# Kernel optimization log

Measured on AMD Instinct MI355X. Metric: run time of the kernel, lower is better.

## Reference

```python
import jax, jax.numpy as jnp
import numpy as np

ALPHA = 0.9
NEG_SLOPE = 0.01  # nn.LeakyReLU default
PAD = 1           # circular padding

def _conv_circular(t, W, b):
    # circular pad spatial dims, then VALID conv (matches padding_mode='circular')
    tp = jnp.pad(t, ((0, 0), (0, 0), (PAD, PAD), (PAD, PAD)), mode='wrap')
    y = jax.lax.conv_general_dilated(
        tp, W, window_strides=(1, 1), padding='VALID',
        dimension_numbers=('NCHW', 'OIHW', 'NCHW'))
    return y + b[None, :, None, None]

def setup_inputs() -> dict:
    key = jax.random.key(0)
    k1, k2, k3, k4 = jax.random.split(key, 4)
    x = jax.random.normal(k1, (32, 64, 56, 56), dtype=jnp.float32)
    n = jax.random.normal(k2, (32, 64, 56, 56), dtype=jnp.float32)
    fan_in = 64 * 3 * 3
    W = jax.random.normal(k3, (256, 64, 3, 3), dtype=jnp.float32) / np.sqrt(fan_in)
    b = jax.random.normal(k4, (256,), dtype=jnp.float32) * 0.01
    return {"x": x, "n": n, "W": W, "b": b}

def reference(x, n, W, b):
    h1 = _conv_circular(x, W, b)            # [B, N, C, F]
    hn = _conv_circular(n, W, b)            # [B, N, C, F]
    B, N, C, F = h1.shape
    xf = h1.reshape(B, N, C * F)            # tran(x) again == h1
    nf = hn.reshape(B, N, C * F)
    a = jnp.einsum('bnf,bmf->bnm', xf, nf)  # [B, N, M]
    a = jnp.where(a >= 0, a, NEG_SLOPE * a) # LeakyReLU
    attn = jax.nn.softmax(a, axis=1)        # Softmax(dim=1): over rows
    agg = jnp.einsum('bnm,bmf->bnf', attn, xf).reshape(B, N, C, F)
    return (1.0 - ALPHA) * agg + ALPHA * h1
```

## Files before the change

kernel.cpp:

```cpp
#include <hip/hip_runtime.h>
#include <hip/hip_bf16.h>
#include <cstddef>

#define SP 3136
#define CIN 64
#define COUT 256
#define NB 32
#define NEG_SLOPE 0.01f

typedef __attribute__((ext_vector_type(8))) short short8v;
typedef __attribute__((ext_vector_type(4))) float f32x4;

__device__ __forceinline__ float bfr(ushort h) {
    union { uint u; float f; } c; c.u = ((uint)h) << 16; return c.f;
}
__device__ __forceinline__ ushort bf_hi(float v) {
    __hip_bfloat16 h = __float2bfloat16(v);
    return *(ushort*)&h;
}

#define SWZ(row, g) ((((g) ^ ((row) & 7))) * 8)

#define GLOAD_LDS(gp, lp) __builtin_amdgcn_global_load_lds(                    \
    (const __attribute__((address_space(1))) void*)(gp),                       \
    (__attribute__((address_space(3))) void*)(lp), 16, 0, 0)

__global__ __launch_bounds__(256)
void pack_w(const float* __restrict__ W, ushort* __restrict__ wh)
{
    const int id = blockIdx.x * 256 + threadIdx.x;
    const int ci = id & 63, co = (id >> 6) & 255, tap = id >> 14;
    float v = W[(size_t)(co * 64 + ci) * 9 + tap];
    const int ks = ci >> 5, cig = (ci >> 3) & 3, ce = ci & 7;
    const size_t o = (((size_t)(tap * 2 + ks) * 4 + cig) * 256 + co) * 8 + ce;
    wh[o] = bf_hi(v);
}

__global__ __launch_bounds__(256, 2)
void conv_fused(const float* __restrict__ xsrc, const float* __restrict__ nsrc,
                const ushort* __restrict__ Wf_hi,
                const float* __restrict__ bias,
                ushort* __restrict__ h1h, ushort* __restrict__ hnh)
{
    __shared__ __align__(16) ushort Bh[4 * 58 * 64];
    const int tid = threadIdx.x;
    const int w = tid >> 6, l = tid & 63;
    const int bid = blockIdx.x;
    const int xcd = bid & 7, s = bid >> 3;
    const int rp  = s % 28;
    const int img = xcd + 8 * (s / 28);
    const int imgb = img & (NB - 1);
    const int y0 = rp * 2, p0 = rp * 112;
    const int co_w = w * 64;
    const bool isX = (img < NB);

    const float* __restrict__ src = (isX ? xsrc : nsrc) + (size_t)imgb * CIN * SP;
    ushort* __restrict__ dh = (isX ? h1h : hnh) + (size_t)imgb * COUT * SP;

    int sy[4];
    #pragma unroll
    for (int j = 0; j < 4; ++j) sy[j] = (y0 + 55 + j) % 56;

    {
        const int ci = tid >> 2, seg = tid & 3;
        #pragma unroll
        for (int j = 0; j < 4; ++j) {
            const float* r = src + (size_t)ci * SP + sy[j] * 56 + seg * 14;
            #pragma unroll
            for (int c = 0; c < 14; ++c) {
                const int x = seg * 14 + c + 1;
                const int idx = ((j * 58 + x) << 6) + (((ci >> 3) ^ (x & 7)) << 3) + (ci & 7);
                Bh[idx] = bf_hi(r[c]);
            }
        }
        #pragma unroll
        for (int s2 = 0; s2 < 2; ++s2) {
            const int slot = tid * 2 + s2;
            const int j2 = slot >> 7, ci2 = (slot >> 1) & 63, side = slot & 1;
            const float* r2 = src + (size_t)ci2 * SP + sy[j2] * 56;
            const float v = side ? r2[0] : r2[55];
            const int x = side ? 57 : 0;
            const int idx = ((j2 * 58 + x) << 6) + (((ci2 >> 3) ^ (x & 7)) << 3) + (ci2 & 7);
            Bh[idx] = bf_hi(v);
        }
    }
    __syncthreads();

    f32x4 acc[4][7];
    {
        const int rr = (l >> 4) * 4;
        #pragma unroll
        for (int m = 0; m < 4; ++m) {
            const int cb = co_w + 16 * m + rr;
            f32x4 bv = { bias[cb], bias[cb + 1], bias[cb + 2], bias[cb + 3] };
            #pragma unroll
            for (int nf = 0; nf < 7; ++nf) acc[m][nf] = bv;
        }
    }

    int b58[7], bx[7];
    #pragma unroll
    for (int nf = 0; nf < 7; ++nf) {
        const int sp = nf * 16 + (l & 15);
        const int ry = (sp >= 56) ? 1 : 0;
        const int xx = sp - ry * 56;
        b58[nf] = ry * 58 + xx;
        bx[nf]  = xx;
    }

    size_t aoff[4];
    #pragma unroll
    for (int m = 0; m < 4; ++m)
        aoff[m] = ((size_t)(l >> 4) * 256 + co_w + 16 * m + (l & 15)) * 8;

    short8v cah[4];
    #pragma unroll
    for (int m = 0; m < 4; ++m)
        cah[m] = *(const short8v*)(Wf_hi + aoff[m]);

    for (int it = 0; it < 18; ++it) {
        const int tap = it >> 1, ks = it & 1;
        const int dy = tap / 3, dx = tap - dy * 3;
        const int toff = dy * 58 + dx;
        const int grp = ks * 4 + (l >> 4);

        short8v nah[4];
        {
            const size_t po = (size_t)(it < 17 ? it + 1 : it) * 8192;
            #pragma unroll
            for (int m = 0; m < 4; ++m)
                nah[m] = *(const short8v*)(Wf_hi + aoff[m] + po);
        }

        #pragma unroll
        for (int nf = 0; nf < 7; ++nf) {
            const int x  = bx[nf] + dx;
            const int bi = ((b58[nf] + toff) << 6) + ((grp ^ (x & 7)) << 3);
            short8v bh = *(const short8v*)&Bh[bi];
            #pragma unroll
            for (int m = 0; m < 4; ++m)
                acc[m][nf] = __builtin_amdgcn_mfma_f32_16x16x32_bf16(cah[m], bh, acc[m][nf], 0, 0, 0);
        }
        #pragma unroll
        for (int m = 0; m < 4; ++m) cah[m] = nah[m];
    }

    const int rr = (l >> 4) * 4, cc = l & 15;
    #pragma unroll
    for (int m = 0; m < 4; ++m) {
        const int cb = co_w + 16 * m + rr;
        #pragma unroll
        for (int nf = 0; nf < 7; ++nf) {
            const int p = p0 + nf * 16 + cc;
            #pragma unroll
            for (int r = 0; r < 4; ++r)
                dh[(size_t)(cb + r) * SP + p] = bf_hi(acc[m][nf][r]);
        }
    }
}

__global__ __launch_bounds__(256, 2)
void gemm_a_mfma(const ushort* __restrict__ h1h, const ushort* __restrict__ hnh,
                 float* __restrict__ attn)
{
    __shared__ __align__(16) ushort Ah[64][64];
    __shared__ __align__(16) ushort Bh[64][64];
    const int tid = threadIdx.x;
    const int w = tid >> 6, l = tid & 63;
    const int wn = w >> 1, wm = w & 1;
    const int bid = blockIdx.x;
    const int xcd = bid & 7, s = bid >> 3;
    const int tile = s % 16;
    const int img  = xcd + 8 * (s / 16);
    const int n0 = (tile & 3) * 64, m0 = (tile >> 2) * 64;

    const ushort* __restrict__ mat0 = h1h + ((size_t)img * COUT + n0) * SP;
    const ushort* __restrict__ mat1 = hnh + ((size_t)img * COUT + m0) * SP;

    f32x4 acc[2][2];
    #pragma unroll
    for (int i = 0; i < 2; ++i)
        #pragma unroll
        for (int j = 0; j < 2; ++j) acc[i][j] = (f32x4){0.f, 0.f, 0.f, 0.f};

    const int lr = l >> 3, gp = l & 7;
    const int glog = gp ^ lr;
    const ushort* gptr[4];
    ushort* lptr[4];
    #pragma unroll
    for (int t = 0; t < 4; ++t) {
        const int u = 4 * w + t, mat = u >> 3, seg = u & 7;
        const ushort* ms = (mat == 0) ? mat0 : mat1;
        ushort* lb = (mat == 0) ? &Ah[0][0] : &Bh[0][0];
        gptr[t] = ms + (size_t)(seg * 8 + lr) * SP + glog * 8;
        lptr[t] = lb + seg * 8 * 64;
    }

    for (int k0 = 0; k0 < SP; k0 += 64) {
        #pragma unroll
        for (int t = 0; t < 4; ++t)
            GLOAD_LDS(gptr[t] + k0, lptr[t]);
        __syncthreads();

        #pragma unroll
        for (int ks = 0; ks < 2; ++ks) {
            const int grp = ks * 4 + (l >> 4);
            short8v ahf[2], bhf[2];
            #pragma unroll
            for (int i = 0; i < 2; ++i) {
                const int ar_ = 32 * wn + 16 * i + (l & 15);
                ahf[i] = *(const short8v*)&Ah[ar_][SWZ(ar_, grp)];
                const int br_ = 32 * wm + 16 * i + (l & 15);
                bhf[i] = *(const short8v*)&Bh[br_][SWZ(br_, grp)];
            }
            #pragma unroll
            for (int i = 0; i < 2; ++i)
                #pragma unroll
                for (int j = 0; j < 2; ++j)
                    acc[i][j] = __builtin_amdgcn_mfma_f32_16x16x32_bf16(ahf[i], bhf[j], acc[i][j], 0, 0, 0);
        }
        __syncthreads();
    }

    const int rr = (l >> 4) * 4, cc = l & 15;
    float* __restrict__ aimg = attn + (size_t)img * COUT * COUT;
    #pragma unroll
    for (int i = 0; i < 2; ++i) {
        const int nb = n0 + 32 * wn + 16 * i + rr;
        #pragma unroll
        for (int j = 0; j < 2; ++j) {
            const int m = m0 + 32 * wm + 16 * j + cc;
            #pragma unroll
            for (int r = 0; r < 4; ++r) {
                float v = acc[i][j][r];
                v = (v >= 0.f) ? v : NEG_SLOPE * v;
                aimg[(size_t)(nb + r) * COUT + m] = v;
            }
        }
    }
}

__global__ __launch_bounds__(64)
void softmax_k(float* __restrict__ attn)
{
    const int b = blockIdx.y;
    const int m = blockIdx.x * 64 + threadIdx.x;
    float* a = attn + (size_t)b * COUT * COUT;
    float mx = -1e30f;
    for (int n_ = 0; n_ < COUT; ++n_) mx = fmaxf(mx, a[n_ * COUT + m]);
    float s = 0.f;
    for (int n_ = 0; n_ < COUT; ++n_) s += expf(a[n_ * COUT + m] - mx);
    float inv = 1.f / s;
    for (int n_ = 0; n_ < COUT; ++n_)
        a[n_ * COUT + m] = expf(a[n_ * COUT + m] - mx) * inv;
}

__global__ __launch_bounds__(256, 4)
void gemm_agg_mfma(const float* __restrict__ attn,
                   const ushort* __restrict__ h1h,
                   float* __restrict__ out)
{
    __shared__ __align__(16) ushort Ah[128][72];
    __shared__ __align__(16) ushort Bh[112][72];
    const int tid = threadIdx.x, w = tid >> 6, l = tid & 63;
    const int f0 = blockIdx.x * 112;
    const int n0 = blockIdx.y * 128;
    const int img = blockIdx.z;

    const float*  __restrict__ A  = attn + (size_t)img * COUT * COUT;
    const ushort* __restrict__ Hh = h1h + (size_t)img * COUT * SP;

    f32x4 acc[2][7];
    #pragma unroll
    for (int nf = 0; nf < 2; ++nf)
        #pragma unroll
        for (int mf = 0; mf < 7; ++mf) acc[nf][mf] = (f32x4){0.f, 0.f, 0.f, 0.f};

    const int ar = tid >> 1, ac = (tid & 1) * 32;
    const int bm = tid >> 2, bq = tid & 3, bfo = bq * 28;

    for (int k0 = 0; k0 < COUT; k0 += 64) {
        {
            const float* g = A + (size_t)(n0 + ar) * COUT + k0 + ac;
            uint* dh = (uint*)&Ah[ar][ac];
            #pragma unroll
            for (int q = 0; q < 8; ++q) {
                float4 v = *(const float4*)(g + 4 * q);
                dh[2 * q]     = (uint)bf_hi(v.x) | ((uint)bf_hi(v.y) << 16);
                dh[2 * q + 1] = (uint)bf_hi(v.z) | ((uint)bf_hi(v.w) << 16);
            }
        }
        {
            const ushort* g = Hh + (size_t)(k0 + bm) * SP + f0 + bfo;
            #pragma unroll
            for (int e = 0; e < 7; ++e) {
                uint2 v = *(const uint2*)(g + 4 * e);
                const ushort* vp = (const ushort*)&v;
                #pragma unroll
                for (int j = 0; j < 4; ++j)
                    Bh[bfo + 4 * e + j][bm] = vp[j];
            }
        }
        __syncthreads();
        #pragma unroll
        for (int ks = 0; ks < 2; ++ks) {
            const int kb = ks * 32 + (l >> 4) * 8;
            short8v ah[2];
            #pragma unroll
            for (int nf = 0; nf < 2; ++nf) {
                const int row = 32 * w + 16 * nf + (l & 15);
                ah[nf] = *(const short8v*)&Ah[row][kb];
            }
            #pragma unroll
            for (int mf = 0; mf < 7; ++mf) {
                const int br = mf * 16 + (l & 15);
                short8v bh = *(const short8v*)&Bh[br][kb];
                #pragma unroll
                for (int nf = 0; nf < 2; ++nf)
                    acc[nf][mf] = __builtin_amdgcn_mfma_f32_16x16x32_bf16(ah[nf], bh, acc[nf][mf], 0, 0, 0);
            }
        }
        __syncthreads();
    }

    const int rr = (l >> 4) * 4, cc = l & 15;
    float* __restrict__ orow = out + (size_t)img * COUT * SP;
    #pragma unroll
    for (int nf = 0; nf < 2; ++nf) {
        const int nb = n0 + 32 * w + 16 * nf + rr;
        #pragma unroll
        for (int mf = 0; mf < 7; ++mf) {
            const int f = f0 + 16 * mf + cc;
            #pragma unroll
            for (int r = 0; r < 4; ++r) {
                const int n = nb + r;
                float h = bfr(Hh[(size_t)n * SP + f]);
                orow[(size_t)n * SP + f] = 0.1f * acc[nf][mf][r] + 0.9f * h;
            }
        }
    }
}

extern "C" void kernel_launch(void* const* d_in, const int* in_sizes, int n_in,
                              void* d_out, int out_size, void* d_ws, size_t ws_size,
                              hipStream_t stream)
{
    const float* x    = (const float*)d_in[0];
    const float* nn   = (const float*)d_in[1];
    const float* W    = (const float*)d_in[2];
    const float* bias = (const float*)d_in[3];
    float* out = (float*)d_out;

    ushort* h1b_hi = (ushort*)d_ws;
    char*   zone   = (char*)(h1b_hi + (size_t)NB * COUT * SP);
    ushort* Wf_hi  = (ushort*)zone;
    float*  attn   = (float*)zone;
    ushort* hnb_hi = (ushort*)d_out;

    pack_w    <<<576, 256, 0, stream>>>(W, Wf_hi);
    conv_fused<<<1792, 256, 0, stream>>>(x, nn, Wf_hi, bias, h1b_hi, hnb_hi);
    gemm_a_mfma  <<<512, 256, 0, stream>>>(h1b_hi, hnb_hi, attn);
    softmax_k    <<<dim3(4, NB),     64,  0, stream>>>(attn);
    gemm_agg_mfma<<<dim3(28, 2, NB), 256, 0, stream>>>(attn, h1b_hi, out);
}
```

Baseline: 245.2 us.

## Emit bf16 softmax output and stream it into LDS with direct global loads

The softmax kernel now writes its normalized weights as bf16 into a separate buffer instead of overwriting the fp32 attention matrix in place. The aggregation GEMM loads that bf16 A tile straight into a swizzled LDS layout with global_load_lds, replacing the per-thread fp32 load, convert and store. Its 1D grid is also remapped so all tiles of one image land on the same XCD, which should improve L2 reuse of that image's data. The cost is extra workspace for the bf16 buffer and new swizzle indexing; the padded Bh row width also changes.

```diff
diff --git a/kernel.cpp b/kernel.cpp
--- a/kernel.cpp
+++ b/kernel.cpp
@@ -241,33 +241,37 @@
 }
 
 __global__ __launch_bounds__(64)
-void softmax_k(float* __restrict__ attn)
+void softmax_k(const float* __restrict__ attn, ushort* __restrict__ attnb)
 {
     const int b = blockIdx.y;
     const int m = blockIdx.x * 64 + threadIdx.x;
-    float* a = attn + (size_t)b * COUT * COUT;
+    const float* a = attn + (size_t)b * COUT * COUT;
+    ushort* ab = attnb + (size_t)b * COUT * COUT;
     float mx = -1e30f;
     for (int n_ = 0; n_ < COUT; ++n_) mx = fmaxf(mx, a[n_ * COUT + m]);
     float s = 0.f;
     for (int n_ = 0; n_ < COUT; ++n_) s += expf(a[n_ * COUT + m] - mx);
     float inv = 1.f / s;
     for (int n_ = 0; n_ < COUT; ++n_)
-        a[n_ * COUT + m] = expf(a[n_ * COUT + m] - mx) * inv;
+        ab[n_ * COUT + m] = bf_hi(expf(a[n_ * COUT + m] - mx) * inv);
 }
 
 __global__ __launch_bounds__(256, 4)
-void gemm_agg_mfma(const float* __restrict__ attn,
+void gemm_agg_mfma(const ushort* __restrict__ attnb,
                    const ushort* __restrict__ h1h,
                    float* __restrict__ out)
 {
-    __shared__ __align__(16) ushort Ah[128][72];
-    __shared__ __align__(16) ushort Bh[112][72];
+    __shared__ __align__(16) ushort Ah[128][64];
+    __shared__ __align__(16) ushort Bh[112][76];
     const int tid = threadIdx.x, w = tid >> 6, l = tid & 63;
-    const int f0 = blockIdx.x * 112;
-    const int n0 = blockIdx.y * 128;
-    const int img = blockIdx.z;
-
-    const float*  __restrict__ A  = attn + (size_t)img * COUT * COUT;
+    const int bid = blockIdx.x;
+    const int xcd = bid & 7, s = bid >> 3;
+    const int local = s % 56;
+    const int img  = xcd + 8 * (s / 56);
+    const int f0 = (local % 28) * 112;
+    const int n0 = (local / 28) * 128;
+
+    const ushort* __restrict__ A  = attnb + (size_t)img * COUT * COUT;
     const ushort* __restrict__ Hh = h1h + (size_t)img * COUT * SP;
 
     f32x4 acc[2][7];
@@ -276,20 +280,22 @@
         #pragma unroll
         for (int mf = 0; mf < 7; ++mf) acc[nf][mf] = (f32x4){0.f, 0.f, 0.f, 0.f};
 
-    const int ar = tid >> 1, ac = (tid & 1) * 32;
+    const int lr = l >> 3, gp = l & 7;
+    const int glog = gp ^ lr;
+    const ushort* agp[4];
+    ushort* alp[4];
+    #pragma unroll
+    for (int t = 0; t < 4; ++t) {
+        const int seg = 4 * w + t;
+        agp[t] = A + (size_t)(n0 + seg * 8 + lr) * COUT + glog * 8;
+        alp[t] = &Ah[0][0] + seg * 8 * 64;
+    }
     const int bm = tid >> 2, bq = tid & 3, bfo = bq * 28;
 
     for (int k0 = 0; k0 < COUT; k0 += 64) {
-        {
-            const float* g = A + (size_t)(n0 + ar) * COUT + k0 + ac;
-            uint* dh = (uint*)&Ah[ar][ac];
-            #pragma unroll
-            for (int q = 0; q < 8; ++q) {
-                float4 v = *(const float4*)(g + 4 * q);
-                dh[2 * q]     = (uint)bf_hi(v.x) | ((uint)bf_hi(v.y) << 16);
-                dh[2 * q + 1] = (uint)bf_hi(v.z) | ((uint)bf_hi(v.w) << 16);
-            }
-        }
+        #pragma unroll
+        for (int t = 0; t < 4; ++t)
+            GLOAD_LDS(agp[t] + k0, alp[t]);
         {
             const ushort* g = Hh + (size_t)(k0 + bm) * SP + f0 + bfo;
             #pragma unroll
@@ -304,12 +310,13 @@
         __syncthreads();
         #pragma unroll
         for (int ks = 0; ks < 2; ++ks) {
+            const int grp = ks * 4 + (l >> 4);
             const int kb = ks * 32 + (l >> 4) * 8;
             short8v ah[2];
             #pragma unroll
             for (int nf = 0; nf < 2; ++nf) {
                 const int row = 32 * w + 16 * nf + (l & 15);
-                ah[nf] = *(const short8v*)&Ah[row][kb];
+                ah[nf] = *(const short8v*)&Ah[row][SWZ(row, grp)];
             }
             #pragma unroll
             for (int mf = 0; mf < 7; ++mf) {
@@ -355,11 +362,12 @@
     char*   zone   = (char*)(h1b_hi + (size_t)NB * COUT * SP);
     ushort* Wf_hi  = (ushort*)zone;
     float*  attn   = (float*)zone;
+    ushort* attnb  = (ushort*)(zone + (size_t)NB * COUT * COUT * sizeof(float));
     ushort* hnb_hi = (ushort*)d_out;
 
     pack_w    <<<576, 256, 0, stream>>>(W, Wf_hi);
     conv_fused<<<1792, 256, 0, stream>>>(x, nn, Wf_hi, bias, h1b_hi, hnb_hi);
     gemm_a_mfma  <<<512, 256, 0, stream>>>(h1b_hi, hnb_hi, attn);
-    softmax_k    <<<dim3(4, NB),     64,  0, stream>>>(attn);
-    gemm_agg_mfma<<<dim3(28, 2, NB), 256, 0, stream>>>(attn, h1b_hi, out);
-}
+    softmax_k    <<<dim3(4, NB), 64, 0, stream>>>(attn, attnb);
+    gemm_agg_mfma<<<1792, 256, 0, stream>>>(attnb, h1b_hi, out);
+}
```

Result: faster. 196.8 us (-19.7%).
